# Optimization experiments

Measured on AMD Instinct MI355X. Metric: run time of the kernel, lower is better.

Reference implementation:

```python
import jax, jax.numpy as jnp
import numpy as np

D = 2048; N_H = 16; D_H = 128; D_R = 64; FFN = 8192
THETA = 1000000.0; EPS = 1e-6
SCALE = 1.0 / np.sqrt(D_H + D_R)


def rms_norm(x, w):
    xf = x.astype(jnp.float32)
    n = jax.lax.rsqrt(jnp.mean(xf * xf, axis=-1, keepdims=True) + EPS)
    return (xf * n).astype(x.dtype) * w


def build_rope_cache(seq_len, dim):
    freqs = 1.0 / (THETA ** (jnp.arange(0, dim, 2, dtype=jnp.float32) / dim))
    f = jnp.arange(seq_len, dtype=jnp.float32)[:, None] * freqs[None, :]  # (S, dim/2)
    cos = jnp.repeat(jnp.cos(f), 2, axis=-1)  # (S, dim)
    sin = jnp.repeat(jnp.sin(f), 2, axis=-1)
    return cos, sin


def apply_rope(x, cos, sin):
    # x: (B, H, S, d); cos/sin: (S, d)
    x1 = x[..., ::2]
    x2 = x[..., 1::2]
    x_rot = jnp.stack([-x2, x1], axis=-1).reshape(x.shape)
    return x * cos + x_rot * sin


def setup_inputs() -> dict:
    key = jax.random.key(0)
    ks = jax.random.split(key, 16)
    B, M, N = 2, 2048, 2048
    s = 0.02
    return {
        "query": jax.random.normal(ks[0], (B, M, D), jnp.float32),
        "key_value": jax.random.normal(ks[1], (B, N, D), jnp.float32),
        "g_q": jnp.ones((D,), jnp.float32),
        "g_kv": jnp.ones((D,), jnp.float32),
        "g_ffn": jnp.ones((D,), jnp.float32),
        "w_qc": jax.random.normal(ks[2], (D, N_H * D_H), jnp.float32) * s,
        "w_kc": jax.random.normal(ks[3], (D, N_H * D_H), jnp.float32) * s,
        "w_qr": jax.random.normal(ks[4], (D, N_H * D_R), jnp.float32) * s,
        "w_kr": jax.random.normal(ks[5], (D, N_H * D_R), jnp.float32) * s,
        "w_v": jax.random.normal(ks[6], (D, N_H * D_H), jnp.float32) * s,
        "w_o": jax.random.normal(ks[7], (N_H * D_H, D), jnp.float32) * s,
        "w_gate": jax.random.normal(ks[8], (D, FFN), jnp.float32) * s,
        "w_up": jax.random.normal(ks[9], (D, FFN), jnp.float32) * s,
        "w_down": jax.random.normal(ks[10], (FFN, D), jnp.float32) * s,
    }


def reference(query, key_value, g_q, g_kv, g_ffn, w_qc, w_kc, w_qr, w_kr, w_v, w_o, w_gate, w_up, w_down):
    B, M, _ = query.shape
    N = key_value.shape[1]

    qn = rms_norm(query, g_q)
    kvn = rms_norm(key_value, g_kv)

    Q_C = (qn @ w_qc).reshape(B, M, N_H, D_H).transpose(0, 2, 1, 3)   # bhmd
    K_C = (kvn @ w_kc).reshape(B, N, N_H, D_H).transpose(0, 2, 1, 3)  # bhnd
    Q_R = (qn @ w_qr).reshape(B, M, N_H, D_R).transpose(0, 2, 1, 3)
    K_R = (kvn @ w_kr).reshape(B, N, N_H, D_R).transpose(0, 2, 1, 3)
    V = (kvn @ w_v).reshape(B, N, N_H, D_H).transpose(0, 2, 1, 3)

    cos, sin = build_rope_cache(max(M, N), D_R)
    Q_R = apply_rope(Q_R, cos[:M], sin[:M])
    K_R = apply_rope(K_R, cos[:N], sin[:N])

    scores = (jnp.einsum('bhmd,bhnd->bhmn', Q_C, K_C)
              + jnp.einsum('bhmr,bhnr->bhmn', Q_R, K_R)) * SCALE
    attn = jax.nn.softmax(scores, axis=-1)
    out = jnp.einsum('bhmn,bhnd->bhmd', attn, V)
    out = out.transpose(0, 2, 1, 3).reshape(B, M, N_H * D_H)
    attn_out = out @ w_o

    x = query + attn_out
    xn = rms_norm(x, g_ffn)
    ffn_out = (jax.nn.silu(xn @ w_gate) * (xn @ w_up)) @ w_down
    return x + ffn_out
```

## Files before the change

### kernel.cpp

```cpp
#include <hip/hip_runtime.h>
#include <stdint.h>


typedef unsigned short u16;
typedef __bf16 bf16x8 __attribute__((ext_vector_type(8)));
typedef unsigned short u16x8 __attribute__((ext_vector_type(8)));
typedef unsigned short u16x4 __attribute__((ext_vector_type(4)));
typedef float f32x4 __attribute__((ext_vector_type(4)));

#define LOG2E 1.4426950408889634f
#define SCALE_F 0.07216878364870323f

__device__ __forceinline__ f32x4 mfma16(bf16x8 a, bf16x8 b, f32x4 c) {
  return __builtin_amdgcn_mfma_f32_16x16x32_bf16(a, b, c, 0, 0, 0);
}

__device__ __forceinline__ u16 f2bf(float f) {
  union { float f; unsigned u; } x; x.f = f;
  unsigned r = x.u + 0x7fffu + ((x.u >> 16) & 1u);
  return (u16)(r >> 16);
}
__device__ __forceinline__ float bf2f(u16 v) {
  union { unsigned u; float f; } x; x.u = ((unsigned)v) << 16;
  return x.f;
}

__device__ __forceinline__ void gload_lds16(const u16* g, u16* l) {
  __builtin_amdgcn_global_load_lds(
      (const __attribute__((address_space(1))) unsigned int*)g,
      (__attribute__((address_space(3))) unsigned int*)l, 16, 0, 0);
}

__global__ __launch_bounds__(256) void rmsnorm_k(const float* __restrict__ x,
                                                 const float* __restrict__ g,
                                                 u16* __restrict__ out) {
  const int row = blockIdx.x;
  const int t = threadIdx.x;
  const float* xr = x + (size_t)row * 2048;
  float4 a = ((const float4*)xr)[t * 2];
  float4 b = ((const float4*)xr)[t * 2 + 1];
  float ss = a.x*a.x + a.y*a.y + a.z*a.z + a.w*a.w
           + b.x*b.x + b.y*b.y + b.z*b.z + b.w*b.w;
  #pragma unroll
  for (int off = 32; off; off >>= 1) ss += __shfl_xor(ss, off, 64);
  __shared__ float w4[4];
  if ((t & 63) == 0) w4[t >> 6] = ss;
  __syncthreads();
  ss = w4[0] + w4[1] + w4[2] + w4[3];
  const float n = rsqrtf(ss * (1.0f / 2048.0f) + 1e-6f);
  const float* gr = g + t * 8;
  u16x8 o;
  o[0] = f2bf(a.x * n * gr[0]); o[1] = f2bf(a.y * n * gr[1]);
  o[2] = f2bf(a.z * n * gr[2]); o[3] = f2bf(a.w * n * gr[3]);
  o[4] = f2bf(b.x * n * gr[4]); o[5] = f2bf(b.y * n * gr[5]);
  o[6] = f2bf(b.z * n * gr[6]); o[7] = f2bf(b.w * n * gr[7]);
  *(u16x8*)&out[(size_t)row * 2048 + t * 8] = o;
}

__global__ __launch_bounds__(256) void conv_t(const float* __restrict__ in,
                                              u16* __restrict__ out,
                                              int R, int C, int ldin) {
  __shared__ float tile[64][65];
  const int r0 = blockIdx.y * 64, c0 = blockIdx.x * 64;
  const int tr = threadIdx.x >> 6, tc = threadIdx.x & 63;
  #pragma unroll
  for (int i = 0; i < 16; ++i) {
    int rr = tr * 16 + i;
    tile[rr][tc] = in[(size_t)(r0 + rr) * ldin + c0 + tc];
  }
  __syncthreads();
  #pragma unroll
  for (int i = 0; i < 16; ++i) {
    int rr = tr * 16 + i;
    out[(size_t)(c0 + rr) * R + r0 + tc] = f2bf(tile[tc][rr]);
  }
}

__global__ __launch_bounds__(256) void transpose_bf16(const u16* __restrict__ in,
                                                      u16* __restrict__ out,
                                                      int R, int C) {
  __shared__ u16 tile[64][65];
  const size_t zoff = (size_t)blockIdx.z * R * C;
  const u16* inz = in + zoff;
  u16* outz = out + zoff;
  const int r0 = blockIdx.y * 64, c0 = blockIdx.x * 64;
  const int tr = threadIdx.x >> 6, tc = threadIdx.x & 63;
  #pragma unroll
  for (int i = 0; i < 16; ++i) {
    int rr = tr * 16 + i;
    tile[rr][tc] = inz[(size_t)(r0 + rr) * C + c0 + tc];
  }
  __syncthreads();
  #pragma unroll
  for (int i = 0; i < 16; ++i) {
    int rr = tr * 16 + i;
    outz[(size_t)(c0 + rr) * R + r0 + tc] = tile[tc][rr];
  }
}

__global__ __launch_bounds__(256) void rope_k(u16* __restrict__ buf) {
  const int idx = blockIdx.x * 256 + threadIdx.x;
  const int i = idx & 31;
  const int pos = (idx >> 5) & 2047;
  const int bh = idx >> 16;
  u16* p = buf + ((size_t)(bh * 2048 + pos)) * 192 + 128 + 2 * i;
  const float inv = exp2f(-(float)(2 * i) * (19.931568569324174f / 64.0f));
  const float f = (float)pos * inv;
  const float c = cosf(f), s = sinf(f);
  const float x1 = bf2f(p[0]), x2 = bf2f(p[1]);
  p[0] = f2bf(x1 * c - x2 * s);
  p[1] = f2bf(x2 * c + x1 * s);
}

template <int EPI>
__global__ __launch_bounds__(256) void gemm_bt(const u16* __restrict__ A,
                                               const u16* __restrict__ Bt,
                                               int N, int K,
                                               void* __restrict__ outp,
                                               const void* __restrict__ auxp) {
  __shared__ __attribute__((aligned(16))) u16 As[128 * 32];
  __shared__ __attribute__((aligned(16))) u16 Bs[128 * 32];
  const int t = threadIdx.x;
  const int wv = t >> 6, quad = (t >> 4) & 3, ln = t & 15;
  const int lane = t & 63;
  const int bm0 = blockIdx.y * 128, bn0 = blockIdx.x * 128;
  const int wm = (wv >> 1) * 64, wn = (wv & 1) * 64;

  f32x4 acc[4][4] = {};

  const int r_in = lane >> 2;
  const int c_in = (lane & 3) * 8;

  for (int kk = 0; kk < K; kk += 32) {
    #pragma unroll
    for (int i = 0; i < 2; ++i) {
      const int row = (i * 4 + wv) * 16 + r_in;
      gload_lds16(&A[(size_t)(bm0 + row) * K + kk + c_in], &As[row * 32 + c_in]);
      gload_lds16(&Bt[(size_t)(bn0 + row) * K + kk + c_in], &Bs[row * 32 + c_in]);
    }
    __syncthreads();
    bf16x8 af[4], bfr[4];
    #pragma unroll
    for (int mt = 0; mt < 4; ++mt)
      af[mt] = *(const bf16x8*)&As[(wm + mt * 16 + ln) * 32 + quad * 8];
    #pragma unroll
    for (int nt = 0; nt < 4; ++nt)
      bfr[nt] = *(const bf16x8*)&Bs[(wn + nt * 16 + ln) * 32 + quad * 8];
    #pragma unroll
    for (int mt = 0; mt < 4; ++mt)
      #pragma unroll
      for (int nt = 0; nt < 4; ++nt)
        acc[mt][nt] = mfma16(af[mt], bfr[nt], acc[mt][nt]);
    __syncthreads();
  }

  #pragma unroll
  for (int mt = 0; mt < 4; ++mt) {
    #pragma unroll
    for (int r = 0; r < 4; ++r) {
      const int gm = bm0 + wm + mt * 16 + quad * 4 + r;
      #pragma unroll
      for (int nt = 0; nt < 4; ++nt) {
        const int gn = bn0 + wn + nt * 16 + ln;
        float v = acc[mt][nt][r];
        if constexpr (EPI == 0) {
          ((u16*)outp)[(size_t)gm * N + gn] = f2bf(v);
        } else if constexpr (EPI >= 1 && EPI <= 4) {
          if constexpr (EPI == 1 || EPI == 2) v *= SCALE_F * LOG2E;
          const int bb = gm >> 11, mm = gm & 2047;
          int h, d, off;
          if constexpr (EPI == 1 || EPI == 3) { h = gn >> 7; d = gn & 127; off = 0; }
          else                                { h = gn >> 6; d = gn & 63; off = 128; }
          ((u16*)outp)[((size_t)((bb * 16 + h) * 2048 + mm)) * 192 + off + d] = f2bf(v);
        } else if constexpr (EPI == 5) {
          const int bb = gm >> 11, mm = gm & 2047;
          const int h = gn >> 7, d = gn & 127;
          ((u16*)outp)[((size_t)((bb * 16 + h) * 2048 + mm)) * 128 + d] = f2bf(v);
        } else if constexpr (EPI == 6) {
          ((float*)outp)[(size_t)gm * N + gn] =
              v + ((const float*)auxp)[(size_t)gm * N + gn];
        } else if constexpr (EPI == 7) {
          const float g = bf2f(((const u16*)auxp)[(size_t)gm * N + gn]);
          const float s = g / (1.0f + __expf(-g));
          ((u16*)outp)[(size_t)gm * N + gn] = f2bf(s * v);
        }
      }
    }
  }
}

__global__ __launch_bounds__(256, 2) void flash_k(const u16* __restrict__ Q,
                                                  const u16* __restrict__ K,
                                                  const u16* __restrict__ VT,
                                                  u16* __restrict__ O) {
  __shared__ __attribute__((aligned(16))) u16 Ks[2][64 * 192];
  __shared__ __attribute__((aligned(16))) u16 Vs[128 * 64];

  const int t = threadIdx.x;
  const int wv = t >> 6, quad = (t >> 4) & 3, ln = t & 15;
  const int lane = t & 63;
  const int b = blockIdx.z, h = blockIdx.y;
  const int m0 = blockIdx.x * 128;
  const size_t qbase = ((size_t)(b * 16 + h)) * 2048;
  const u16* kg = K + qbase * 192;
  const u16* vg = VT + ((size_t)(b * 16 + h)) * 128 * 2048;

  int krow[6], kscol[6];
  #pragma unroll
  for (int i = 0; i < 6; ++i) {
    const int o = (wv * 6 + i) * 1024 + lane * 16;
    const int r = o / 384;
    const int c = o - r * 384;
    krow[i] = r;
    kscol[i] = c ^ ((r & 7) << 4);
  }
  int vrow[4], vscol[4];
  #pragma unroll
  for (int i = 0; i < 4; ++i) {
    const int o = (wv * 4 + i) * 1024 + lane * 16;
    const int r = o >> 7;
    vrow[i] = r;
    vscol[i] = (o & 127) ^ ((r & 7) << 4);
  }

  bf16x8 qfA[6], qfB[6];
  {
    const u16* qpA = Q + (qbase + m0 + wv * 16 + ln) * 192 + quad * 8;
    const u16* qpB = qpA + 64 * 192;
    #pragma unroll
    for (int ks = 0; ks < 6; ++ks) {
      qfA[ks] = *(const bf16x8*)&qpA[ks * 32];
      qfB[ks] = *(const bf16x8*)&qpB[ks * 32];
    }
  }

  float mA = -1e30f, lA = 0.0f, mB = -1e30f, lB = 0.0f;
  f32x4 ofA[8] = {}, ofB[8] = {};

  #pragma unroll
  for (int i = 0; i < 6; ++i)
    gload_lds16(kg + (size_t)krow[i] * 192 + (kscol[i] >> 1),
                &Ks[0][(wv * 6 + i) * 512 + lane * 8]);
  #pragma unroll
  for (int i = 0; i < 4; ++i)
    gload_lds16(vg + (size_t)vrow[i] * 2048 + (vscol[i] >> 1),
                &Vs[(wv * 4 + i) * 512 + lane * 8]);
  __syncthreads();

  int cur = 0;
  for (int j = 0; j < 32; ++j) {
    if (j < 31) {
      #pragma unroll
      for (int i = 0; i < 6; ++i)
        gload_lds16(kg + (size_t)((j + 1) * 64 + krow[i]) * 192 + (kscol[i] >> 1),
                    &Ks[cur ^ 1][(wv * 6 + i) * 512 + lane * 8]);
    }

    f32x4 sA[4], sB[4];
    #pragma unroll
    for (int nt = 0; nt < 4; ++nt) {
      f32x4 za = {0.f, 0.f, 0.f, 0.f}, zb = {0.f, 0.f, 0.f, 0.f};
      const int row = nt * 16 + ln;
      const u16* kr = &Ks[cur][row * 192];
      const int sw = (row & 7) << 4;
      #pragma unroll
      for (int ks = 0; ks < 6; ++ks) {
        bf16x8 kb = *(const bf16x8*)&kr[((ks * 64 + quad * 16) ^ sw) >> 1];
        za = mfma16(kb, qfA[ks], za);
        zb = mfma16(kb, qfB[ks], zb);
      }
      sA[nt] = za; sB[nt] = zb;
    }

    float mxA = sA[0][0], mxB = sB[0][0];
    #pragma unroll
    for (int nt = 0; nt < 4; ++nt)
      #pragma unroll
      for (int r = 0; r < 4; ++r) {
        mxA = fmaxf(mxA, sA[nt][r]);
        mxB = fmaxf(mxB, sB[nt][r]);
      }
    mxA = fmaxf(mxA, __shfl_xor(mxA, 16, 64));
    mxA = fmaxf(mxA, __shfl_xor(mxA, 32, 64));
    mxB = fmaxf(mxB, __shfl_xor(mxB, 16, 64));
    mxB = fmaxf(mxB, __shfl_xor(mxB, 32, 64));

    if (__any((mxA > mA + 11.0f) || (mxB > mB + 11.0f))) {
      const float mnA = fmaxf(mA, mxA), mnB = fmaxf(mB, mxB);
      const float aA = exp2f(mA - mnA), aB = exp2f(mB - mnB);
      mA = mnA; mB = mnB;
      lA *= aA; lB *= aB;
      #pragma unroll
      for (int dt = 0; dt < 8; ++dt)
        #pragma unroll
        for (int r = 0; r < 4; ++r) {
          ofA[dt][r] *= aA;
          ofB[dt][r] *= aB;
        }
    }

    float rsA = 0.0f, rsB = 0.0f;
    #pragma unroll
    for (int nt = 0; nt < 4; ++nt)
      #pragma unroll
      for (int r = 0; r < 4; ++r) {
        const float pa = exp2f(sA[nt][r] - mA);
        const float pb = exp2f(sB[nt][r] - mB);
        sA[nt][r] = pa; sB[nt][r] = pb;
        rsA += pa; rsB += pb;
      }
    rsA += __shfl_xor(rsA, 16, 64);
    rsA += __shfl_xor(rsA, 32, 64);
    rsB += __shfl_xor(rsB, 16, 64);
    rsB += __shfl_xor(rsB, 32, 64);
    lA += rsA; lB += rsB;

    unsigned pkA[4][2], pkB[4][2];
    #pragma unroll
    for (int nt = 0; nt < 4; ++nt) {
      pkA[nt][0] = (unsigned)f2bf(sA[nt][0]) | ((unsigned)f2bf(sA[nt][1]) << 16);
      pkA[nt][1] = (unsigned)f2bf(sA[nt][2]) | ((unsigned)f2bf(sA[nt][3]) << 16);
      pkB[nt][0] = (unsigned)f2bf(sB[nt][0]) | ((unsigned)f2bf(sB[nt][1]) << 16);
      pkB[nt][1] = (unsigned)f2bf(sB[nt][2]) | ((unsigned)f2bf(sB[nt][3]) << 16);
    }
    unsigned pawA[2][4], pawB[2][4];
    #pragma unroll
    for (int kt = 0; kt < 2; ++kt)
      #pragma unroll
      for (int w = 0; w < 4; ++w) {
        const int src = ((quad & 1) * 2 + (w >> 1)) * 16 + ln;
        const int loA = __shfl((int)pkA[2 * kt][w & 1], src, 64);
        const int hiA = __shfl((int)pkA[2 * kt + 1][w & 1], src, 64);
        pawA[kt][w] = (unsigned)((quad & 2) ? hiA : loA);
        const int loB = __shfl((int)pkB[2 * kt][w & 1], src, 64);
        const int hiB = __shfl((int)pkB[2 * kt + 1][w & 1], src, 64);
        pawB[kt][w] = (unsigned)((quad & 2) ? hiB : loB);
      }

    __syncthreads();

    #pragma unroll
    for (int kt = 0; kt < 2; ++kt) {
      union { unsigned u[4]; bf16x8 b; } paA, paB;
      #pragma unroll
      for (int w = 0; w < 4; ++w) { paA.u[w] = pawA[kt][w]; paB.u[w] = pawB[kt][w]; }
      #pragma unroll
      for (int dt = 0; dt < 8; ++dt) {
        const int row = dt * 16 + ln;
        const int sw = (row & 7) << 4;
        bf16x8 vb = *(const bf16x8*)&Vs[row * 64 +
                                        (((kt * 64 + quad * 16) ^ sw) >> 1)];
        ofA[dt] = mfma16(vb, paA.b, ofA[dt]);
        ofB[dt] = mfma16(vb, paB.b, ofB[dt]);
      }
    }

    __syncthreads();

    if (j < 31) {
      #pragma unroll
      for (int i = 0; i < 4; ++i)
        gload_lds16(vg + (size_t)vrow[i] * 2048 + (j + 1) * 64 + (vscol[i] >> 1),
                    &Vs[(wv * 4 + i) * 512 + lane * 8]);
    }
    cur ^= 1;
  }

  const float invA = 1.0f / lA, invB = 1.0f / lB;
  #pragma unroll
  for (int dt = 0; dt < 8; ++dt) {
    u16x4 oa, ob;
    #pragma unroll
    for (int r = 0; r < 4; ++r) {
      oa[r] = f2bf(ofA[dt][r] * invA);
      ob[r] = f2bf(ofB[dt][r] * invB);
    }
    *(u16x4*)&O[((size_t)(b * 2048 + m0 + wv * 16 + ln)) * 2048 +
                h * 128 + dt * 16 + quad * 4] = oa;
    *(u16x4*)&O[((size_t)(b * 2048 + m0 + 64 + wv * 16 + ln)) * 2048 +
                h * 128 + dt * 16 + quad * 4] = ob;
  }
}

extern "C" void kernel_launch(void* const* d_in, const int* in_sizes, int n_in,
                              void* d_out, int out_size, void* d_ws, size_t ws_size,
                              hipStream_t stream) {
  const float* query     = (const float*)d_in[0];
  const float* key_value = (const float*)d_in[1];
  const float* g_q       = (const float*)d_in[2];
  const float* g_kv      = (const float*)d_in[3];
  const float* g_ffn     = (const float*)d_in[4];
  const float* w_qc      = (const float*)d_in[5];
  const float* w_kc      = (const float*)d_in[6];
  const float* w_qr      = (const float*)d_in[7];
  const float* w_kr      = (const float*)d_in[8];
  const float* w_v       = (const float*)d_in[9];
  const float* w_o       = (const float*)d_in[10];
  const float* w_gate    = (const float*)d_in[11];
  const float* w_up      = (const float*)d_in[12];
  const float* w_down    = (const float*)d_in[13];

  char* ws = (char*)d_ws;
  const size_t MiB = 1048576;
  u16*   qn   = (u16*)(ws + 0 * MiB);
  u16*   kvn  = (u16*)(ws + 16 * MiB);
  u16*   Qb   = (u16*)(ws + 32 * MiB);
  u16*   Kb   = (u16*)(ws + 56 * MiB);
  u16*   Vb   = (u16*)(ws + 80 * MiB);
  u16*   wt   = (u16*)(ws + 96 * MiB);
  u16*   VT   = (u16*)(ws + 0 * MiB);
  u16*   attn = (u16*)(ws + 16 * MiB);
  float* x    = (float*)(ws + 64 * MiB);
  u16*   xn   = (u16*)(ws + 0 * MiB);
  u16*   ghalf= (u16*)(ws + 16 * MiB);
  u16*   wtf  = (u16*)(ws + 48 * MiB);

  const dim3 blk(256);

  rmsnorm_k<<<4096, blk, 0, stream>>>(query, g_q, qn);
  rmsnorm_k<<<4096, blk, 0, stream>>>(key_value, g_kv, kvn);

  conv_t<<<dim3(32, 32), blk, 0, stream>>>(w_qc, wt, 2048, 2048, 2048);
  gemm_bt<1><<<dim3(16, 32), blk, 0, stream>>>(qn, wt, 2048, 2048, Qb, nullptr);
  conv_t<<<dim3(16, 32), blk, 0, stream>>>(w_qr, wt, 2048, 1024, 1024);
  gemm_bt<2><<<dim3(8, 32), blk, 0, stream>>>(qn, wt, 1024, 2048, Qb, nullptr);
  conv_t<<<dim3(32, 32), blk, 0, stream>>>(w_kc, wt, 2048, 2048, 2048);
  gemm_bt<3><<<dim3(16, 32), blk, 0, stream>>>(kvn, wt, 2048, 2048, Kb, nullptr);
  conv_t<<<dim3(16, 32), blk, 0, stream>>>(w_kr, wt, 2048, 1024, 1024);
  gemm_bt<4><<<dim3(8, 32), blk, 0, stream>>>(kvn, wt, 1024, 2048, Kb, nullptr);
  conv_t<<<dim3(32, 32), blk, 0, stream>>>(w_v, wt, 2048, 2048, 2048);
  gemm_bt<5><<<dim3(16, 32), blk, 0, stream>>>(kvn, wt, 2048, 2048, Vb, nullptr);

  rope_k<<<8192, blk, 0, stream>>>(Qb);
  rope_k<<<8192, blk, 0, stream>>>(Kb);

  transpose_bf16<<<dim3(2, 32, 32), blk, 0, stream>>>(Vb, VT, 2048, 128);

  flash_k<<<dim3(16, 16, 2), blk, 0, stream>>>(Qb, Kb, VT, attn);

  conv_t<<<dim3(32, 32), blk, 0, stream>>>(w_o, wt, 2048, 2048, 2048);
  gemm_bt<6><<<dim3(16, 32), blk, 0, stream>>>(attn, wt, 2048, 2048, x, query);

  rmsnorm_k<<<4096, blk, 0, stream>>>(x, g_ffn, xn);
  for (int h = 0; h < 2; ++h) {
    const int n0 = h * 4096;
    conv_t<<<dim3(64, 32), blk, 0, stream>>>(w_gate + n0, wtf, 2048, 4096, 8192);
    gemm_bt<0><<<dim3(32, 32), blk, 0, stream>>>(xn, wtf, 4096, 2048, ghalf, nullptr);
    conv_t<<<dim3(64, 32), blk, 0, stream>>>(w_up + n0, wtf, 2048, 4096, 8192);
    gemm_bt<7><<<dim3(32, 32), blk, 0, stream>>>(xn, wtf, 4096, 2048, ghalf, ghalf);
    conv_t<<<dim3(32, 64), blk, 0, stream>>>(w_down + (size_t)n0 * 2048, wtf,
                                             4096, 2048, 2048);
    gemm_bt<6><<<dim3(16, 32), blk, 0, stream>>>(ghalf, wtf, 2048, 4096,
                                                 (float*)d_out,
                                                 h == 0 ? (const void*)x
                                                        : (const void*)d_out);
  }
}
```

Before: 1.464 ms.

## Deepen GEMM K-tile to 64 with XOR-swizzled LDS, grouped block order, packed bf16 cvt

The GEMM now stages a 64-wide K slice per iteration instead of 32, which halves the number of barrier pairs. It stores the tiles in LDS with an XOR swizzle on the 16-byte column chunk to avoid bank conflicts on the fragment reads. Block indices are remapped so consecutive blocks are spread across eight groups, which changes L2 and XCD locality. The attention kernel packs its probabilities using the hardware v_cvt_pk_bf16_f32 instruction in place of manual rounding. The trade-off is doubled LDS use per block, and the swizzle mapping assumes the grid size is divisible by 8.

```diff
diff --git a/kernel.cpp b/kernel.cpp
--- a/kernel.cpp
+++ b/kernel.cpp
@@ -23,6 +23,11 @@
 __device__ __forceinline__ float bf2f(u16 v) {
   union { unsigned u; float f; } x; x.u = ((unsigned)v) << 16;
   return x.f;
+}
+__device__ __forceinline__ unsigned cvt_pk_bf16(float lo, float hi) {
+  unsigned r;
+  asm("v_cvt_pk_bf16_f32 %0, %1, %2" : "=v"(r) : "v"(lo), "v"(hi));
+  return r;
 }
 
 __device__ __forceinline__ void gload_lds16(const u16* g, u16* l) {
@@ -118,39 +123,59 @@
                                                int N, int K,
                                                void* __restrict__ outp,
                                                const void* __restrict__ auxp) {
-  __shared__ __attribute__((aligned(16))) u16 As[128 * 32];
-  __shared__ __attribute__((aligned(16))) u16 Bs[128 * 32];
+  __shared__ __attribute__((aligned(16))) u16 As[128 * 64];
+  __shared__ __attribute__((aligned(16))) u16 Bs[128 * 64];
   const int t = threadIdx.x;
   const int wv = t >> 6, quad = (t >> 4) & 3, ln = t & 15;
-  const int lane = t & 63;
-  const int bm0 = blockIdx.y * 128, bn0 = blockIdx.x * 128;
+
+  const int nbx = gridDim.x;
+  const int lin = blockIdx.y * nbx + blockIdx.x;
+  const int cpx = (nbx * gridDim.y) >> 3;
+  const int swz = (lin & 7) * cpx + (lin >> 3);
+  const int bm0 = (swz / nbx) * 128, bn0 = (swz % nbx) * 128;
   const int wm = (wv >> 1) * 64, wn = (wv & 1) * 64;
 
   f32x4 acc[4][4] = {};
 
-  const int r_in = lane >> 2;
-  const int c_in = (lane & 3) * 8;
-
-  for (int kk = 0; kk < K; kk += 32) {
-    #pragma unroll
-    for (int i = 0; i < 2; ++i) {
-      const int row = (i * 4 + wv) * 16 + r_in;
-      gload_lds16(&A[(size_t)(bm0 + row) * K + kk + c_in], &As[row * 32 + c_in]);
-      gload_lds16(&Bt[(size_t)(bn0 + row) * K + kk + c_in], &Bs[row * 32 + c_in]);
+  int srow[4], scol[4];
+  #pragma unroll
+  for (int i = 0; i < 4; ++i) {
+    const int row = i * 32 + (t >> 3);
+    const int cB = ((t & 7) * 16) ^ ((row & 7) << 4);
+    srow[i] = row;
+    scol[i] = cB >> 1;
+  }
+
+  for (int kk = 0; kk < K; kk += 64) {
+    #pragma unroll
+    for (int i = 0; i < 4; ++i) {
+      gload_lds16(&A[(size_t)(bm0 + srow[i]) * K + kk + scol[i]],
+                  &As[i * 2048 + t * 8]);
+      gload_lds16(&Bt[(size_t)(bn0 + srow[i]) * K + kk + scol[i]],
+                  &Bs[i * 2048 + t * 8]);
     }
     __syncthreads();
-    bf16x8 af[4], bfr[4];
-    #pragma unroll
-    for (int mt = 0; mt < 4; ++mt)
-      af[mt] = *(const bf16x8*)&As[(wm + mt * 16 + ln) * 32 + quad * 8];
-    #pragma unroll
-    for (int nt = 0; nt < 4; ++nt)
-      bfr[nt] = *(const bf16x8*)&Bs[(wn + nt * 16 + ln) * 32 + quad * 8];
-    #pragma unroll
-    for (int mt = 0; mt < 4; ++mt)
-      #pragma unroll
-      for (int nt = 0; nt < 4; ++nt)
-        acc[mt][nt] = mfma16(af[mt], bfr[nt], acc[mt][nt]);
+    #pragma unroll
+    for (int ks = 0; ks < 2; ++ks) {
+      bf16x8 af[4], bfr[4];
+      #pragma unroll
+      for (int mt = 0; mt < 4; ++mt) {
+        const int row = wm + mt * 16 + ln;
+        af[mt] = *(const bf16x8*)&As[row * 64 +
+                   (((ks * 64 + quad * 16) ^ ((row & 7) << 4)) >> 1)];
+      }
+      #pragma unroll
+      for (int nt = 0; nt < 4; ++nt) {
+        const int row = wn + nt * 16 + ln;
+        bfr[nt] = *(const bf16x8*)&Bs[row * 64 +
+                   (((ks * 64 + quad * 16) ^ ((row & 7) << 4)) >> 1)];
+      }
+      #pragma unroll
+      for (int mt = 0; mt < 4; ++mt)
+        #pragma unroll
+        for (int nt = 0; nt < 4; ++nt)
+          acc[mt][nt] = mfma16(af[mt], bfr[nt], acc[mt][nt]);
+    }
     __syncthreads();
   }
 
@@ -318,10 +343,10 @@
     unsigned pkA[4][2], pkB[4][2];
     #pragma unroll
     for (int nt = 0; nt < 4; ++nt) {
-      pkA[nt][0] = (unsigned)f2bf(sA[nt][0]) | ((unsigned)f2bf(sA[nt][1]) << 16);
-      pkA[nt][1] = (unsigned)f2bf(sA[nt][2]) | ((unsigned)f2bf(sA[nt][3]) << 16);
-      pkB[nt][0] = (unsigned)f2bf(sB[nt][0]) | ((unsigned)f2bf(sB[nt][1]) << 16);
-      pkB[nt][1] = (unsigned)f2bf(sB[nt][2]) | ((unsigned)f2bf(sB[nt][3]) << 16);
+      pkA[nt][0] = cvt_pk_bf16(sA[nt][0], sA[nt][1]);
+      pkA[nt][1] = cvt_pk_bf16(sA[nt][2], sA[nt][3]);
+      pkB[nt][0] = cvt_pk_bf16(sB[nt][0], sB[nt][1]);
+      pkB[nt][1] = cvt_pk_bf16(sB[nt][2], sB[nt][3]);
     }
     unsigned pawA[2][4], pawB[2][4];
     #pragma unroll
```

Measured after the change: 1.330 ms. 1.1x faster.
